# Kernel optimization log

Hardware: AMD Instinct MI355X
Metric: run time of the kernel (lower is better)

Reference implementation:

```python
import jax, jax.numpy as jnp
import numpy as np

CODEBOOK_SIZE = 8192
DIM = 64
B, N = 4, 4096


def setup_inputs() -> dict:
    key = jax.random.key(0)
    k1, k2 = jax.random.split(key)
    x = jax.random.normal(k1, (B, N, DIM), dtype=jnp.float32)
    node_mask = jnp.ones((B, N), dtype=jnp.float32)
    embed = jax.random.normal(k2, (CODEBOOK_SIZE, DIM), dtype=jnp.float32)
    return {"x": x, "node_mask": node_mask, "embed": embed}


def reference(x, node_mask, embed):
    # x: [B, N, D]; embed: [K, D]; node_mask: [B, N]
    b, n, d = x.shape
    k = embed.shape[0]
    flatten = x.reshape(-1, d)  # [B*N, D]
    dist = -(
        jnp.sum(flatten * flatten, axis=1, keepdims=True)
        - 2.0 * (flatten @ embed.T)
        + jnp.sum(embed * embed, axis=1)[None, :]
    )
    embed_ind = jnp.argmax(dist, axis=-1)  # [B*N] nearest-code assignment
    quantize = embed[embed_ind].reshape(b, n, d)  # codebook gather
    # masked one-hot stats (embed_onehot * node_mask), via segment_sum
    mask_flat = node_mask.reshape(-1)
    counts = jax.ops.segment_sum(mask_flat, embed_ind, num_segments=k)  # [K]
    avg_probs = counts / jnp.asarray(flatten.shape[0], dtype=x.dtype)
    perplexity = jnp.exp(-jnp.sum(avg_probs * jnp.log(avg_probs + 1e-10)))
    return quantize, embed_ind.reshape(b, n), perplexity
```

## Files before the change

### kernel.cpp

```cpp
#include <hip/hip_runtime.h>

typedef __attribute__((ext_vector_type(8))) short short8;
typedef __attribute__((ext_vector_type(4))) float f32x4;

#define ROWS 16384
#define DIM 64
#define NCODES 8192
#define MARGIN 0.008f
#define KT_FB 256
#define CTS_PER_BLOCK 32

#define WS_BEST   0
#define WS_COUNTS 131072
#define WS_ENH    163840
#define WS_ESWZ   196608
#define WS_NEED   2293760

__device__ __forceinline__ unsigned long long pack_score(float s, int idx) {
  unsigned u = __float_as_uint(s);
  u ^= (unsigned)((int)u >> 31) | 0x80000000u;
  return ((unsigned long long)u << 32) | (unsigned)(0xFFFF - idx);
}
__device__ __forceinline__ unsigned short bf16hi(float f) {
  unsigned u = __float_as_uint(f);
  return (unsigned short)((u + 0x7FFFu + ((u >> 16) & 1u)) >> 16);
}

__global__ void vq_enorm(const float* __restrict__ embed, float* __restrict__ enh) {
  int k = blockIdx.x * 256 + threadIdx.x;
  const float4* e4 = (const float4*)(embed + (size_t)k * DIM);
  float a = 0.f, b = 0.f, c = 0.f, d = 0.f;
#pragma unroll
  for (int i = 0; i < DIM / 4; ++i) {
    float4 v = e4[i];
    a = fmaf(v.x, v.x, a); b = fmaf(v.y, v.y, b);
    c = fmaf(v.z, v.z, c); d = fmaf(v.w, v.w, d);
  }
  enh[k] = 0.5f * ((a + b) + (c + d));
}

__global__ void vq_prep_e(const float* __restrict__ embed, short* __restrict__ eswz) {
  int u = blockIdx.x * 256 + threadIdx.x;
  int l = u & 63, kc = (u >> 6) & 1, ct = u >> 7;
  int code = ct * 16 + (l & 15);
  int kb = kc * 32 + (l >> 4) * 8;
  const float* er = embed + (size_t)code * DIM + kb;
  short8 h8, l8;
#pragma unroll
  for (int j = 0; j < 8; ++j) {
    float v = er[j];
    unsigned short h = bf16hi(v);
    float r = v - __uint_as_float((unsigned)h << 16);
    h8[j] = (short)h;
    l8[j] = (short)bf16hi(r);
  }
  short8* dst = (short8*)eswz;
  size_t frag = (size_t)ct * 4 + kc * 2;
  dst[(frag + 0) * 64 + l] = h8;
  dst[(frag + 1) * 64 + l] = l8;
}

__global__ __launch_bounds__(256, 4) void vq_screen(
    const float* __restrict__ x, const float* __restrict__ embed,
    const short* __restrict__ eswz, const float* __restrict__ enh,
    unsigned long long* __restrict__ best) {
  const int t = threadIdx.x;
  const int l = t & 63, wid = t >> 6;
  const int cl = l & 15, grp = l >> 4;
  const int row0 = blockIdx.x * 128 + wid * 32;
  const int ct0 = blockIdx.y * CTS_PER_BLOCK;

  short8 ahi[2][2], alo[2][2];
#pragma unroll
  for (int s = 0; s < 2; ++s) {
    const float4* xr4 = (const float4*)(x + (size_t)(row0 + s * 16 + cl) * DIM);
#pragma unroll
    for (int kc = 0; kc < 2; ++kc) {
      const int q = kc * 8 + grp * 2;
      float4 v0 = xr4[q], v1 = xr4[q + 1];
      float vv[8] = {v0.x, v0.y, v0.z, v0.w, v1.x, v1.y, v1.z, v1.w};
#pragma unroll
      for (int j = 0; j < 8; ++j) {
        unsigned short h = bf16hi(vv[j]);
        float r = vv[j] - __uint_as_float((unsigned)h << 16);
        ahi[s][kc][j] = (short)h;
        alo[s][kc][j] = (short)bf16hi(r);
      }
    }
  }

  float bsc[2][4];
  int bidx[2][4];
#pragma unroll
  for (int s = 0; s < 2; ++s)
#pragma unroll
    for (int j = 0; j < 4; ++j) { bsc[s][j] = -3.4e38f; bidx[s][j] = 0; }

  const short8* eb = (const short8*)eswz + (size_t)ct0 * 4 * 64;

  short8 h0 = eb[l], l0 = eb[64 + l], h1 = eb[128 + l], l1 = eb[192 + l];
  float eh = enh[ct0 * 16 + cl];

#pragma unroll
  for (int ci = 0; ci < CTS_PER_BLOCK; ++ci) {
    short8 nh0, nl0, nh1, nl1;
    float neh;
    if (ci + 1 < CTS_PER_BLOCK) {
      const short8* nb = eb + (size_t)(ci + 1) * 256;
      nh0 = nb[l]; nl0 = nb[64 + l]; nh1 = nb[128 + l]; nl1 = nb[192 + l];
      neh = enh[(ct0 + ci + 1) * 16 + cl];
    }

    f32x4 a00 = {-eh, -eh, -eh, -eh};
    f32x4 a10 = a00;
    f32x4 a01 = {0.f, 0.f, 0.f, 0.f};
    f32x4 a11 = a01;
    a00 = __builtin_amdgcn_mfma_f32_16x16x32_bf16(ahi[0][0], h0, a00, 0, 0, 0);
    a10 = __builtin_amdgcn_mfma_f32_16x16x32_bf16(ahi[1][0], h0, a10, 0, 0, 0);
    a01 = __builtin_amdgcn_mfma_f32_16x16x32_bf16(ahi[0][1], h1, a01, 0, 0, 0);
    a11 = __builtin_amdgcn_mfma_f32_16x16x32_bf16(ahi[1][1], h1, a11, 0, 0, 0);
    a00 = __builtin_amdgcn_mfma_f32_16x16x32_bf16(alo[0][0], h0, a00, 0, 0, 0);
    a10 = __builtin_amdgcn_mfma_f32_16x16x32_bf16(alo[1][0], h0, a10, 0, 0, 0);
    a01 = __builtin_amdgcn_mfma_f32_16x16x32_bf16(alo[0][1], h1, a01, 0, 0, 0);
    a11 = __builtin_amdgcn_mfma_f32_16x16x32_bf16(alo[1][1], h1, a11, 0, 0, 0);
    a00 = __builtin_amdgcn_mfma_f32_16x16x32_bf16(ahi[0][0], l0, a00, 0, 0, 0);
    a10 = __builtin_amdgcn_mfma_f32_16x16x32_bf16(ahi[1][0], l0, a10, 0, 0, 0);
    a01 = __builtin_amdgcn_mfma_f32_16x16x32_bf16(ahi[0][1], l1, a01, 0, 0, 0);
    a11 = __builtin_amdgcn_mfma_f32_16x16x32_bf16(ahi[1][1], l1, a11, 0, 0, 0);

    f32x4 s0 = a00 + a01;
    f32x4 s1 = a10 + a11;
    const int code = (ct0 + ci) * 16 + cl;
#pragma unroll
    for (int j = 0; j < 4; ++j) {
      if (s0[j] > bsc[0][j]) { bsc[0][j] = s0[j]; bidx[0][j] = code; }
      if (s1[j] > bsc[1][j]) { bsc[1][j] = s1[j]; bidx[1][j] = code; }
    }

    if (ci + 1 < CTS_PER_BLOCK) {
      h0 = nh0; l0 = nl0; h1 = nh1; l1 = nl1; eh = neh;
    }
  }

  unsigned fmask = 0;
#pragma unroll
  for (int s = 0; s < 2; ++s)
#pragma unroll
    for (int j = 0; j < 4; ++j) {
      float m = bsc[s][j];
      m = fmaxf(m, __shfl_xor(m, 1));
      m = fmaxf(m, __shfl_xor(m, 2));
      m = fmaxf(m, __shfl_xor(m, 4));
      m = fmaxf(m, __shfl_xor(m, 8));
      if (bsc[s][j] >= m - MARGIN) fmask |= 1u << (s * 4 + j);
    }

  float exact[2][4];
#pragma unroll
  for (int s = 0; s < 2; ++s)
#pragma unroll
    for (int j = 0; j < 4; ++j) exact[s][j] = -3.4e38f;

  while (__any((int)(fmask != 0))) {
    const bool act = fmask != 0;
    const int sel = act ? __ffs(fmask) - 1 : 0;
    int code = 0;
#pragma unroll
    for (int s = 0; s < 2; ++s)
#pragma unroll
      for (int j = 0; j < 4; ++j)
        code = (sel == s * 4 + j) ? bidx[s][j] : code;
    int row = act ? (row0 + (sel >> 2) * 16 + grp * 4 + (sel & 3)) : row0;
    if (!act) code = 0;
    const float4* xr = (const float4*)(x + (size_t)row * DIM);
    const float4* er = (const float4*)(embed + (size_t)code * DIM);
    float a0 = 0, a1 = 0, a2 = 0, a3 = 0, n0 = 0, n1 = 0, n2 = 0, n3 = 0;
#pragma unroll
    for (int i = 0; i < 16; ++i) {
      float4 xv = xr[i], ev = er[i];
      a0 = fmaf(xv.x, ev.x, a0); a1 = fmaf(xv.y, ev.y, a1);
      a2 = fmaf(xv.z, ev.z, a2); a3 = fmaf(xv.w, ev.w, a3);
      n0 = fmaf(ev.x, ev.x, n0); n1 = fmaf(ev.y, ev.y, n1);
      n2 = fmaf(ev.z, ev.z, n2); n3 = fmaf(ev.w, ev.w, n3);
    }
    float ex = ((a0 + a1) + (a2 + a3)) - 0.5f * ((n0 + n1) + (n2 + n3));
#pragma unroll
    for (int s = 0; s < 2; ++s)
#pragma unroll
      for (int j = 0; j < 4; ++j)
        exact[s][j] = (act && sel == s * 4 + j) ? ex : exact[s][j];
    fmask = act ? (fmask & (fmask - 1)) : 0u;
  }

#pragma unroll
  for (int s = 0; s < 2; ++s)
#pragma unroll
    for (int j = 0; j < 4; ++j) {
      unsigned long long pk = pack_score(exact[s][j], bidx[s][j]);
      unsigned long long o;
      o = __shfl_xor(pk, 1); pk = pk > o ? pk : o;
      o = __shfl_xor(pk, 2); pk = pk > o ? pk : o;
      o = __shfl_xor(pk, 4); pk = pk > o ? pk : o;
      o = __shfl_xor(pk, 8); pk = pk > o ? pk : o;
      if (cl == 0) atomicMax(&best[row0 + s * 16 + grp * 4 + j], pk);
    }
}

__global__ __launch_bounds__(256, 2) void vq_score_fb(
    const float* __restrict__ x, const float* __restrict__ embed,
    const float* __restrict__ enh, unsigned long long* __restrict__ best) {
  const int row = blockIdx.x * 256 + threadIdx.x;
  const int c0 = blockIdx.y * KT_FB;
  float4 xa[16];
  const float4* xg = (const float4*)(x + (size_t)row * DIM);
#pragma unroll
  for (int i = 0; i < 16; ++i) xa[i] = xg[i];
  float bs = -3.4e38f;
  int bc = 0;
#pragma unroll 2
  for (int c = c0; c < c0 + KT_FB; ++c) {
    const float4* e4 = (const float4*)(embed + (size_t)c * DIM);
    float a0 = 0.f, a1 = 0.f, a2 = 0.f, a3 = 0.f;
#pragma unroll
    for (int i = 0; i < 16; ++i) {
      float4 ev = e4[i];
      a0 = fmaf(xa[i].x, ev.x, a0); a1 = fmaf(xa[i].y, ev.y, a1);
      a2 = fmaf(xa[i].z, ev.z, a2); a3 = fmaf(xa[i].w, ev.w, a3);
    }
    float s = ((a0 + a1) + (a2 + a3)) - enh[c];
    if (s > bs) { bs = s; bc = c; }
  }
  atomicMax(&best[row], pack_score(bs, bc));
}

__global__ void vq_finalize(const unsigned long long* __restrict__ best,
                            const float* __restrict__ embed,
                            const float* __restrict__ node_mask,
                            float* __restrict__ quant,
                            float* __restrict__ out_idx,
                            float* __restrict__ counts) {
  int gid = blockIdx.x * 256 + threadIdx.x;
  int row = gid >> 6, d = gid & 63;
  unsigned long long p = best[row];
  int idx = 0xFFFF - (int)(p & 0xFFFFull);
  quant[gid] = embed[(size_t)idx * DIM + d];
  if (d == 0) {
    out_idx[row] = (float)idx;
    atomicAdd(&counts[idx], node_mask[row]);
  }
}

__global__ void vq_perplexity(const float* __restrict__ counts, float* __restrict__ out) {
  int tid = threadIdx.x;
  float acc = 0.f;
  for (int k = tid; k < NCODES; k += 256) {
    float p = counts[k] * (1.0f / (float)ROWS);
    acc += p * logf(p + 1e-10f);
  }
#pragma unroll
  for (int off = 32; off > 0; off >>= 1) acc += __shfl_down(acc, off);
  __shared__ float red[4];
  if ((tid & 63) == 0) red[tid >> 6] = acc;
  __syncthreads();
  if (tid == 0) out[0] = expf(-((red[0] + red[1]) + (red[2] + red[3])));
}

extern "C" void kernel_launch(void* const* d_in, const int* in_sizes, int n_in,
                              void* d_out, int out_size, void* d_ws, size_t ws_size,
                              hipStream_t stream) {
  const float* x = (const float*)d_in[0];
  const float* node_mask = (const float*)d_in[1];
  const float* embed = (const float*)d_in[2];

  float* out = (float*)d_out;
  float* quant = out;
  float* out_idx = out + (size_t)ROWS * DIM;
  float* out_ppl = out_idx + ROWS;

  unsigned long long* best = (unsigned long long*)((char*)d_ws + WS_BEST);
  float* counts = (float*)((char*)d_ws + WS_COUNTS);
  float* enh = (float*)((char*)d_ws + WS_ENH);
  short* eswz = (short*)((char*)d_ws + WS_ESWZ);

  hipMemsetAsync(d_ws, 0, WS_ENH, stream);
  vq_enorm<<<NCODES / 256, 256, 0, stream>>>(embed, enh);
  if (ws_size >= WS_NEED) {
    vq_prep_e<<<256, 256, 0, stream>>>(embed, eswz);
    vq_screen<<<dim3(ROWS / 128, NCODES / (CTS_PER_BLOCK * 16)), 256, 0, stream>>>(
        x, embed, eswz, enh, best);
  } else {
    vq_score_fb<<<dim3(ROWS / 256, NCODES / KT_FB), 256, 0, stream>>>(x, embed, enh, best);
  }
  vq_finalize<<<ROWS * DIM / 256, 256, 0, stream>>>(best, embed, node_mask, quant, out_idx, counts);
  vq_perplexity<<<1, 256, 0, stream>>>(counts, out_ppl);
}
```

Before: 118.5 us.

## Drop codebook low-half bf16 MFMAs, use norm-based adaptive margin with top-2 rescoring

The screening pass now splits only x into bf16 hi and lo parts and keeps the codebook at a single bf16. That cuts the MFMAs per tile from 12 to 8 and halves the swizzled codebook footprint. To stay correct, each lane tracks the top-2 candidates, and a per-row margin derived from ||x||·max||e|| decides which candidates get an exact fp32 rescore. The risk is a wider margin causing more rescoring work, a looser error bound, plus an extra atomic per code in the norm kernel and a less aggressive prefetch.

```diff
diff --git a/kernel.cpp b/kernel.cpp
--- a/kernel.cpp
+++ b/kernel.cpp
@@ -6,15 +6,15 @@
 #define ROWS 16384
 #define DIM 64
 #define NCODES 8192
-#define MARGIN 0.008f
 #define KT_FB 256
 #define CTS_PER_BLOCK 32
 
 #define WS_BEST   0
 #define WS_COUNTS 131072
-#define WS_ENH    163840
-#define WS_ESWZ   196608
-#define WS_NEED   2293760
+#define WS_EMAX   163840
+#define WS_ENH    164096
+#define WS_ESWZ   196864
+#define WS_NEED   1245440
 
 __device__ __forceinline__ unsigned long long pack_score(float s, int idx) {
   unsigned u = __float_as_uint(s);
@@ -26,7 +26,8 @@
   return (unsigned short)((u + 0x7FFFu + ((u >> 16) & 1u)) >> 16);
 }
 
-__global__ void vq_enorm(const float* __restrict__ embed, float* __restrict__ enh) {
+__global__ void vq_enorm(const float* __restrict__ embed, float* __restrict__ enh,
+                         unsigned* __restrict__ emax2) {
   int k = blockIdx.x * 256 + threadIdx.x;
   const float4* e4 = (const float4*)(embed + (size_t)k * DIM);
   float a = 0.f, b = 0.f, c = 0.f, d = 0.f;
@@ -36,7 +37,9 @@
     a = fmaf(v.x, v.x, a); b = fmaf(v.y, v.y, b);
     c = fmaf(v.z, v.z, c); d = fmaf(v.w, v.w, d);
   }
-  enh[k] = 0.5f * ((a + b) + (c + d));
+  float n2 = (a + b) + (c + d);
+  enh[k] = 0.5f * n2;
+  atomicMax(emax2, __float_as_uint(n2));
 }
 
 __global__ void vq_prep_e(const float* __restrict__ embed, short* __restrict__ eswz) {
@@ -45,25 +48,18 @@
   int code = ct * 16 + (l & 15);
   int kb = kc * 32 + (l >> 4) * 8;
   const float* er = embed + (size_t)code * DIM + kb;
-  short8 h8, l8;
-#pragma unroll
-  for (int j = 0; j < 8; ++j) {
-    float v = er[j];
-    unsigned short h = bf16hi(v);
-    float r = v - __uint_as_float((unsigned)h << 16);
-    h8[j] = (short)h;
-    l8[j] = (short)bf16hi(r);
-  }
-  short8* dst = (short8*)eswz;
-  size_t frag = (size_t)ct * 4 + kc * 2;
-  dst[(frag + 0) * 64 + l] = h8;
-  dst[(frag + 1) * 64 + l] = l8;
-}
+  short8 h8;
+#pragma unroll
+  for (int j = 0; j < 8; ++j) h8[j] = (short)bf16hi(er[j]);
+  ((short8*)eswz)[u] = h8;
+}
+
+#define MFMA16(A, B, C) __builtin_amdgcn_mfma_f32_16x16x32_bf16((A), (B), (C), 0, 0, 0)
 
 __global__ __launch_bounds__(256, 4) void vq_screen(
     const float* __restrict__ x, const float* __restrict__ embed,
     const short* __restrict__ eswz, const float* __restrict__ enh,
-    unsigned long long* __restrict__ best) {
+    const float* __restrict__ emax2, unsigned long long* __restrict__ best) {
   const int t = threadIdx.x;
   const int l = t & 63, wid = t >> 6;
   const int cl = l & 15, grp = l >> 4;
@@ -71,6 +67,7 @@
   const int ct0 = blockIdx.y * CTS_PER_BLOCK;
 
   short8 ahi[2][2], alo[2][2];
+  float xn[2] = {0.f, 0.f};
 #pragma unroll
   for (int s = 0; s < 2; ++s) {
     const float4* xr4 = (const float4*)(x + (size_t)(row0 + s * 16 + cl) * DIM);
@@ -85,60 +82,65 @@
         float r = vv[j] - __uint_as_float((unsigned)h << 16);
         ahi[s][kc][j] = (short)h;
         alo[s][kc][j] = (short)bf16hi(r);
+        xn[s] = fmaf(vv[j], vv[j], xn[s]);
       }
     }
   }
-
-  float bsc[2][4];
-  int bidx[2][4];
-#pragma unroll
-  for (int s = 0; s < 2; ++s)
-#pragma unroll
-    for (int j = 0; j < 4; ++j) { bsc[s][j] = -3.4e38f; bidx[s][j] = 0; }
-
-  const short8* eb = (const short8*)eswz + (size_t)ct0 * 4 * 64;
-
-  short8 h0 = eb[l], l0 = eb[64 + l], h1 = eb[128 + l], l1 = eb[192 + l];
-  float eh = enh[ct0 * 16 + cl];
-
-#pragma unroll
+#pragma unroll
+  for (int s = 0; s < 2; ++s) {
+    xn[s] += __shfl_xor(xn[s], 16);
+    xn[s] += __shfl_xor(xn[s], 32);
+  }
+  const float emax = sqrtf(emax2[0]);
+  float mrg[2];
+#pragma unroll
+  for (int s = 0; s < 2; ++s)
+    mrg[s] = sqrtf(xn[s]) * emax * (2.2f / 256.0f) + 3e-3f;
+
+  float bsc[2][4], psc[2][4];
+  int bidx[2][4], sidx[2][4];
+#pragma unroll
+  for (int s = 0; s < 2; ++s)
+#pragma unroll
+    for (int j = 0; j < 4; ++j) {
+      bsc[s][j] = -3.4e38f; psc[s][j] = -3.4e38f;
+      bidx[s][j] = 0; sidx[s][j] = 0;
+    }
+
+  const short8* eb = (const short8*)eswz + (size_t)ct0 * 2 * 64;
+
+#pragma unroll 2
   for (int ci = 0; ci < CTS_PER_BLOCK; ++ci) {
-    short8 nh0, nl0, nh1, nl1;
-    float neh;
-    if (ci + 1 < CTS_PER_BLOCK) {
-      const short8* nb = eb + (size_t)(ci + 1) * 256;
-      nh0 = nb[l]; nl0 = nb[64 + l]; nh1 = nb[128 + l]; nl1 = nb[192 + l];
-      neh = enh[(ct0 + ci + 1) * 16 + cl];
-    }
+    const short8* bt = eb + (size_t)ci * 128;
+    short8 bh0 = bt[l], bh1 = bt[64 + l];
+    const float eh = enh[(ct0 + ci) * 16 + cl];
 
     f32x4 a00 = {-eh, -eh, -eh, -eh};
     f32x4 a10 = a00;
     f32x4 a01 = {0.f, 0.f, 0.f, 0.f};
     f32x4 a11 = a01;
-    a00 = __builtin_amdgcn_mfma_f32_16x16x32_bf16(ahi[0][0], h0, a00, 0, 0, 0);
-    a10 = __builtin_amdgcn_mfma_f32_16x16x32_bf16(ahi[1][0], h0, a10, 0, 0, 0);
-    a01 = __builtin_amdgcn_mfma_f32_16x16x32_bf16(ahi[0][1], h1, a01, 0, 0, 0);
-    a11 = __builtin_amdgcn_mfma_f32_16x16x32_bf16(ahi[1][1], h1, a11, 0, 0, 0);
-    a00 = __builtin_amdgcn_mfma_f32_16x16x32_bf16(alo[0][0], h0, a00, 0, 0, 0);
-    a10 = __builtin_amdgcn_mfma_f32_16x16x32_bf16(alo[1][0], h0, a10, 0, 0, 0);
-    a01 = __builtin_amdgcn_mfma_f32_16x16x32_bf16(alo[0][1], h1, a01, 0, 0, 0);
-    a11 = __builtin_amdgcn_mfma_f32_16x16x32_bf16(alo[1][1], h1, a11, 0, 0, 0);
-    a00 = __builtin_amdgcn_mfma_f32_16x16x32_bf16(ahi[0][0], l0, a00, 0, 0, 0);
-    a10 = __builtin_amdgcn_mfma_f32_16x16x32_bf16(ahi[1][0], l0, a10, 0, 0, 0);
-    a01 = __builtin_amdgcn_mfma_f32_16x16x32_bf16(ahi[0][1], l1, a01, 0, 0, 0);
-    a11 = __builtin_amdgcn_mfma_f32_16x16x32_bf16(ahi[1][1], l1, a11, 0, 0, 0);
-
-    f32x4 s0 = a00 + a01;
-    f32x4 s1 = a10 + a11;
+    a00 = MFMA16(ahi[0][0], bh0, a00);
+    a10 = MFMA16(ahi[1][0], bh0, a10);
+    a01 = MFMA16(ahi[0][1], bh1, a01);
+    a11 = MFMA16(ahi[1][1], bh1, a11);
+    a00 = MFMA16(alo[0][0], bh0, a00);
+    a10 = MFMA16(alo[1][0], bh0, a10);
+    a01 = MFMA16(alo[0][1], bh1, a01);
+    a11 = MFMA16(alo[1][1], bh1, a11);
+
+    f32x4 s0 = a00 + a01, s1 = a10 + a11;
     const int code = (ct0 + ci) * 16 + cl;
 #pragma unroll
     for (int j = 0; j < 4; ++j) {
-      if (s0[j] > bsc[0][j]) { bsc[0][j] = s0[j]; bidx[0][j] = code; }
-      if (s1[j] > bsc[1][j]) { bsc[1][j] = s1[j]; bidx[1][j] = code; }
-    }
-
-    if (ci + 1 < CTS_PER_BLOCK) {
-      h0 = nh0; l0 = nl0; h1 = nh1; l1 = nl1; eh = neh;
+      float v0 = s0[j], v1 = s1[j];
+      if (v0 > bsc[0][j]) {
+        psc[0][j] = bsc[0][j]; sidx[0][j] = bidx[0][j];
+        bsc[0][j] = v0; bidx[0][j] = code;
+      } else if (v0 > psc[0][j]) { psc[0][j] = v0; sidx[0][j] = code; }
+      if (v1 > bsc[1][j]) {
+        psc[1][j] = bsc[1][j]; sidx[1][j] = bidx[1][j];
+        bsc[1][j] = v1; bidx[1][j] = code;
+      } else if (v1 > psc[1][j]) { psc[1][j] = v1; sidx[1][j] = code; }
     }
   }
 
@@ -152,25 +154,28 @@
       m = fmaxf(m, __shfl_xor(m, 2));
       m = fmaxf(m, __shfl_xor(m, 4));
       m = fmaxf(m, __shfl_xor(m, 8));
-      if (bsc[s][j] >= m - MARGIN) fmask |= 1u << (s * 4 + j);
-    }
-
-  float exact[2][4];
-#pragma unroll
-  for (int s = 0; s < 2; ++s)
-#pragma unroll
-    for (int j = 0; j < 4; ++j) exact[s][j] = -3.4e38f;
+      m -= mrg[s];
+      if (bsc[s][j] >= m) fmask |= 1u << (s * 4 + j);
+      if (psc[s][j] >= m) fmask |= 1u << (s * 4 + j + 8);
+    }
+
+  unsigned long long exactp[2][4];
+#pragma unroll
+  for (int s = 0; s < 2; ++s)
+#pragma unroll
+    for (int j = 0; j < 4; ++j) exactp[s][j] = 0ull;
 
   while (__any((int)(fmask != 0))) {
     const bool act = fmask != 0;
     const int sel = act ? __ffs(fmask) - 1 : 0;
+    const int slot = sel & 7, which = sel >> 3;
     int code = 0;
 #pragma unroll
     for (int s = 0; s < 2; ++s)
 #pragma unroll
       for (int j = 0; j < 4; ++j)
-        code = (sel == s * 4 + j) ? bidx[s][j] : code;
-    int row = act ? (row0 + (sel >> 2) * 16 + grp * 4 + (sel & 3)) : row0;
+        if (slot == s * 4 + j) code = which ? sidx[s][j] : bidx[s][j];
+    int row = act ? (row0 + (slot >> 2) * 16 + grp * 4 + (slot & 3)) : row0;
     if (!act) code = 0;
     const float4* xr = (const float4*)(x + (size_t)row * DIM);
     const float4* er = (const float4*)(embed + (size_t)code * DIM);
@@ -184,11 +189,12 @@
       n2 = fmaf(ev.z, ev.z, n2); n3 = fmaf(ev.w, ev.w, n3);
     }
     float ex = ((a0 + a1) + (a2 + a3)) - 0.5f * ((n0 + n1) + (n2 + n3));
+    unsigned long long cand = act ? pack_score(ex, code) : 0ull;
 #pragma unroll
     for (int s = 0; s < 2; ++s)
 #pragma unroll
       for (int j = 0; j < 4; ++j)
-        exact[s][j] = (act && sel == s * 4 + j) ? ex : exact[s][j];
+        if (slot == s * 4 + j) exactp[s][j] = exactp[s][j] > cand ? exactp[s][j] : cand;
     fmask = act ? (fmask & (fmask - 1)) : 0u;
   }
 
@@ -196,8 +202,7 @@
   for (int s = 0; s < 2; ++s)
 #pragma unroll
     for (int j = 0; j < 4; ++j) {
-      unsigned long long pk = pack_score(exact[s][j], bidx[s][j]);
-      unsigned long long o;
+      unsigned long long pk = exactp[s][j], o;
       o = __shfl_xor(pk, 1); pk = pk > o ? pk : o;
       o = __shfl_xor(pk, 2); pk = pk > o ? pk : o;
       o = __shfl_xor(pk, 4); pk = pk > o ? pk : o;
@@ -279,15 +284,16 @@
 
   unsigned long long* best = (unsigned long long*)((char*)d_ws + WS_BEST);
   float* counts = (float*)((char*)d_ws + WS_COUNTS);
+  unsigned* emax2 = (unsigned*)((char*)d_ws + WS_EMAX);
   float* enh = (float*)((char*)d_ws + WS_ENH);
   short* eswz = (short*)((char*)d_ws + WS_ESWZ);
 
   hipMemsetAsync(d_ws, 0, WS_ENH, stream);
-  vq_enorm<<<NCODES / 256, 256, 0, stream>>>(embed, enh);
+  vq_enorm<<<NCODES / 256, 256, 0, stream>>>(embed, enh, emax2);
   if (ws_size >= WS_NEED) {
     vq_prep_e<<<256, 256, 0, stream>>>(embed, eswz);
     vq_screen<<<dim3(ROWS / 128, NCODES / (CTS_PER_BLOCK * 16)), 256, 0, stream>>>(
-        x, embed, eswz, enh, best);
+        x, embed, eswz, enh, (const float*)emax2, best);
   } else {
     vq_score_fb<<<dim3(ROWS / 256, NCODES / KT_FB), 256, 0, stream>>>(x, embed, enh, best);
   }
```

Result: slower. 159.7 us (+34.7%).
